# Performance work log

Measured on AMD Instinct MI355X. Metric: run time of the kernel, lower is better.

The kernel has to match this reference:

```python
import jax, jax.numpy as jnp
import numpy as np

N = 100000   # nodes
E = 1600000  # edges (avg degree 16)
D = 128      # in = hid = out dim
EPS = 1e-5   # BatchNorm eps


def setup_inputs() -> dict:
    key = jax.random.key(0)
    ks = jax.random.split(key, 14)
    x = jax.random.normal(ks[0], (N, D), dtype=jnp.float32)
    row = jax.random.randint(ks[1], (E,), 0, N, dtype=jnp.int32)
    col = jax.random.randint(ks[2], (E,), 0, N, dtype=jnp.int32)
    edge_weight = jax.random.uniform(ks[3], (E,), dtype=jnp.float32)
    s = 1.0 / np.sqrt(D)
    W0 = jax.random.uniform(ks[4], (D, D), jnp.float32, -s, s)
    b0 = jax.random.uniform(ks[5], (D,), jnp.float32, -s, s)
    W1 = jax.random.uniform(ks[6], (D, D), jnp.float32, -s, s)
    b1 = jax.random.uniform(ks[7], (D,), jnp.float32, -s, s)
    W2 = jax.random.uniform(ks[8], (D, D), jnp.float32, -s, s)
    b2 = jax.random.uniform(ks[9], (D,), jnp.float32, -s, s)
    g0 = jnp.ones((D,), jnp.float32); be0 = jnp.zeros((D,), jnp.float32)
    g1 = jnp.ones((D,), jnp.float32); be1 = jnp.zeros((D,), jnp.float32)
    return {"x": x, "edge_weight": edge_weight,
            "W0": W0, "b0": b0, "g0": g0, "be0": be0,
            "W1": W1, "b1": b1, "g1": g1, "be1": be1,
            "W2": W2, "b2": b2, "row": row, "col": col}


def _spmm(edge_weight, row, col, h):
    # (A_norm @ h) with A in COO: out[r] = sum_e w_e * h[col_e] for row_e == r
    return jax.ops.segment_sum(edge_weight[:, None] * h[col], row, num_segments=N)


def _bn(h, gamma, beta):
    # BatchNorm1d, training-mode stats (biased variance), over the node axis
    m = h.mean(axis=0)
    v = h.var(axis=0)
    return gamma * (h - m) * jax.lax.rsqrt(v + EPS) + beta


def reference(x, edge_weight, W0, b0, g0, be0, W1, b1, g1, be1, W2, b2, row, col):
    # hidden block 1: SpMM(A, Linear(h)) -> BN -> ReLU (dropout p=0)
    h = jax.nn.relu(_bn(_spmm(edge_weight, row, col, x @ W0 + b0), g0, be0))
    # hidden block 2
    h = jax.nn.relu(_bn(_spmm(edge_weight, row, col, h @ W1 + b1), g1, be1))
    # final layer: SpMM(A, Linear(h)), no BN/activation
    return _spmm(edge_weight, row, col, h @ W2 + b2)
```

## Files before the change

kernel.cpp:

```cpp
#include <hip/hip_runtime.h>
#include <cstddef>

#define DD 128
#define EPS 1e-5f

typedef short short8 __attribute__((ext_vector_type(8)));
typedef float float4v __attribute__((ext_vector_type(4)));

__device__ __forceinline__ unsigned short f2bf(float f) {
    union { float f; unsigned int u; } x; x.f = f;
    unsigned int r = x.u + 0x7fffu + ((x.u >> 16) & 1u);
    return (unsigned short)(r >> 16);
}
__device__ __forceinline__ float bfhi2f(unsigned int hi_bits) {
    union { unsigned int u; float f; } x; x.u = hi_bits;
    return x.f;
}


__global__ void hist_kernel(const int* __restrict__ row, int* __restrict__ deg, int E) {
    int e = blockIdx.x * blockDim.x + threadIdx.x;
    if (e < E) atomicAdd(&deg[row[e]], 1);
}

__global__ void scanA_kernel(const int* __restrict__ deg, int* __restrict__ tmp,
                             int* __restrict__ bsum, int n) {
    __shared__ int s[1024];
    int tid = threadIdx.x;
    int gid = blockIdx.x * 1024 + tid;
    int v = (gid < n) ? deg[gid] : 0;
    s[tid] = v;
    __syncthreads();
    for (int off = 1; off < 1024; off <<= 1) {
        int t = s[tid];
        int u = (tid >= off) ? s[tid - off] : 0;
        __syncthreads();
        s[tid] = t + u;
        __syncthreads();
    }
    if (gid < n) tmp[gid] = s[tid];
    if (tid == 1023) bsum[blockIdx.x] = s[1023];
}

__global__ void scanB_kernel(const int* __restrict__ bsum, int* __restrict__ boff,
                             int* __restrict__ row_start, int nb, int n) {
    __shared__ int s[128];
    int tid = threadIdx.x;
    int v = (tid < nb) ? bsum[tid] : 0;
    s[tid] = v;
    __syncthreads();
    for (int off = 1; off < 128; off <<= 1) {
        int t = s[tid];
        int u = (tid >= off) ? s[tid - off] : 0;
        __syncthreads();
        s[tid] = t + u;
        __syncthreads();
    }
    if (tid < nb) boff[tid] = s[tid] - v;
    if (tid == nb - 1) row_start[n] = s[tid];
}

__global__ void scanC_kernel(const int* __restrict__ deg, const int* __restrict__ tmp,
                             const int* __restrict__ boff, int* __restrict__ row_start,
                             int* __restrict__ cursor, int n) {
    int gid = blockIdx.x * 1024 + threadIdx.x;
    if (gid < n) {
        int rs = tmp[gid] - deg[gid] + boff[blockIdx.x];
        row_start[gid] = rs;
        cursor[gid] = rs;
    }
}

#define SCHUNK 2048

__global__ __launch_bounds__(256) void scatter_bucketed_kernel(
    const int* __restrict__ row, const int* __restrict__ col,
    const float* __restrict__ ew, int* __restrict__ cursor,
    unsigned long long* __restrict__ ebuf, int E, unsigned int bmagic) {
    int chunk = blockIdx.x >> 3;
    unsigned int bucket = blockIdx.x & 7;
    int base = chunk * SCHUNK + threadIdx.x;
    #pragma unroll
    for (int i = 0; i < SCHUNK / 256; ++i) {
        int e = base + i * 256;
        if (e < E) {
            int r = row[e];
            if (__umulhi((unsigned int)r, bmagic) == bucket) {
                int p = atomicAdd(&cursor[r], 1);
                unsigned long long pk = (unsigned long long)(unsigned int)col[e]
                                      | ((unsigned long long)__float_as_uint(ew[e]) << 32);
                ebuf[p] = pk;
            }
        }
    }
}


__global__ void convw_kernel(const float* __restrict__ W0, const float* __restrict__ W1,
                             const float* __restrict__ W2, unsigned short* __restrict__ T0,
                             unsigned short* __restrict__ T1, unsigned short* __restrict__ T2) {
    const float* W = (blockIdx.y == 0) ? W0 : (blockIdx.y == 1) ? W1 : W2;
    unsigned short* T = (blockIdx.y == 0) ? T0 : (blockIdx.y == 1) ? T1 : T2;
    int gid = blockIdx.x * 256 + threadIdx.x;
    int k = gid >> 7, n = gid & 127;
    T[n * DD + k] = f2bf(W[k * DD + n]);
}


__global__ __launch_bounds__(256) void gemm_mfma_f32_kernel(
    const float* __restrict__ A, const unsigned short* __restrict__ Wt,
    const float* __restrict__ bias, unsigned short* __restrict__ H, int nrows)
{
    __shared__ unsigned short Asl[64][136];
    __shared__ unsigned short Wsl[128][136];

    const int tid  = threadIdx.x;
    const int row0 = blockIdx.x * 64;

    for (int i = tid; i < 2048; i += 256) {
        int r = i >> 4, off = (i & 15) * 8;
        *(uint4*)&Wsl[r][off] = *(const uint4*)(Wt + (size_t)r * DD + off);
    }
    for (int i = tid; i < 2048; i += 256) {
        int r = i >> 5, off4 = i & 31;
        int grow = row0 + r;
        float4 v = make_float4(0.f, 0.f, 0.f, 0.f);
        if (grow < nrows)
            v = *(const float4*)(A + (size_t)grow * DD + off4 * 4);
        ushort4 p;
        p.x = f2bf(v.x); p.y = f2bf(v.y); p.z = f2bf(v.z); p.w = f2bf(v.w);
        *(ushort4*)&Asl[r][off4 * 4] = p;
    }
    __syncthreads();

    const int w = tid >> 6, lane = tid & 63;
    const int m = lane & 15, q = lane >> 4;

    short8 afr[4];
    #pragma unroll
    for (int c = 0; c < 4; ++c)
        afr[c] = *(const short8*)&Asl[w * 16 + m][c * 32 + q * 8];

    float4v acc[8];
    #pragma unroll
    for (int t = 0; t < 8; ++t) acc[t] = (float4v){0.f, 0.f, 0.f, 0.f};

    #pragma unroll
    for (int t = 0; t < 8; ++t) {
        #pragma unroll
        for (int c = 0; c < 4; ++c) {
            short8 bfr = *(const short8*)&Wsl[t * 16 + m][c * 32 + q * 8];
            acc[t] = __builtin_amdgcn_mfma_f32_16x16x32_bf16(afr[c], bfr, acc[t], 0, 0, 0);
        }
    }

    #pragma unroll
    for (int t = 0; t < 8; ++t) {
        float bv = bias[t * 16 + m];
        #pragma unroll
        for (int i = 0; i < 4; ++i)
            Asl[w * 16 + q * 4 + i][t * 16 + m] = f2bf(acc[t][i] + bv);
    }
    __syncthreads();

    for (int i = tid; i < 1024; i += 256) {
        int r = i >> 4, off = (i & 15) * 8;
        if (row0 + r < nrows)
            *(uint4*)(H + (size_t)(row0 + r) * DD + off) = *(const uint4*)&Asl[r][off];
    }
}


__global__ __launch_bounds__(256) void gemm_mfma_bf16_kernel(
    const unsigned int* __restrict__ A, const unsigned short* __restrict__ Wt,
    const float* __restrict__ bias,
    const float* __restrict__ sums, const float* __restrict__ g,
    const float* __restrict__ be,
    unsigned short* __restrict__ H, int nrows)
{
    __shared__ unsigned short Asl[64][136];
    __shared__ unsigned short Wsl[128][136];
    __shared__ float scl_s[128], sft_s[128];

    const int tid  = threadIdx.x;
    const int row0 = blockIdx.x * 64;

    if (tid < 128) {
        float inv_n = 1.0f / (float)nrows;
        float mean = sums[tid] * inv_n;
        float var = sums[128 + tid] * inv_n - mean * mean;
        float rstd = rsqrtf(var + EPS);
        float sc = g[tid] * rstd;
        scl_s[tid] = sc;
        sft_s[tid] = be[tid] - mean * sc;
    }

    for (int i = tid; i < 2048; i += 256) {
        int r = i >> 4, off = (i & 15) * 8;
        *(uint4*)&Wsl[r][off] = *(const uint4*)(Wt + (size_t)r * DD + off);
    }
    __syncthreads();

    for (int i = tid; i < 1024; i += 256) {
        int r = i >> 4, ch = (i & 15) * 8;
        int grow = row0 + r;
        uint4 u = make_uint4(0, 0, 0, 0);
        if (grow < nrows)
            u = *(const uint4*)(A + (size_t)grow * 64 + (ch >> 1));
        unsigned int uu[4] = {u.x, u.y, u.z, u.w};
        unsigned int outp[4];
        #pragma unroll
        for (int j = 0; j < 4; ++j) {
            float vx = bfhi2f(uu[j] << 16);
            float vy = bfhi2f(uu[j] & 0xffff0000u);
            int k = ch + j * 2;
            vx = fmaxf(0.f, vx * scl_s[k] + sft_s[k]);
            vy = fmaxf(0.f, vy * scl_s[k + 1] + sft_s[k + 1]);
            outp[j] = (unsigned int)f2bf(vx) | ((unsigned int)f2bf(vy) << 16);
        }
        *(uint4*)&Asl[r][ch] = *(const uint4*)outp;
    }
    __syncthreads();

    const int w = tid >> 6, lane = tid & 63;
    const int m = lane & 15, q = lane >> 4;

    short8 afr[4];
    #pragma unroll
    for (int c = 0; c < 4; ++c)
        afr[c] = *(const short8*)&Asl[w * 16 + m][c * 32 + q * 8];

    float4v acc[8];
    #pragma unroll
    for (int t = 0; t < 8; ++t) acc[t] = (float4v){0.f, 0.f, 0.f, 0.f};

    #pragma unroll
    for (int t = 0; t < 8; ++t) {
        #pragma unroll
        for (int c = 0; c < 4; ++c) {
            short8 bfr = *(const short8*)&Wsl[t * 16 + m][c * 32 + q * 8];
            acc[t] = __builtin_amdgcn_mfma_f32_16x16x32_bf16(afr[c], bfr, acc[t], 0, 0, 0);
        }
    }

    #pragma unroll
    for (int t = 0; t < 8; ++t) {
        float bv = bias[t * 16 + m];
        #pragma unroll
        for (int i = 0; i < 4; ++i)
            Asl[w * 16 + q * 4 + i][t * 16 + m] = f2bf(acc[t][i] + bv);
    }
    __syncthreads();

    for (int i = tid; i < 1024; i += 256) {
        int r = i >> 4, off = (i & 15) * 8;
        if (row0 + r < nrows)
            *(uint4*)(H + (size_t)(row0 + r) * DD + off) = *(const uint4*)&Asl[r][off];
    }
}


__global__ __launch_bounds__(256) void spmm_bf16_kernel(
    const unsigned short* __restrict__ H, const int* __restrict__ row_start,
    const unsigned long long* __restrict__ ebuf,
    float* __restrict__ Sf, unsigned int* __restrict__ Sb, int writeBF, int N)
{
    int g = threadIdx.x >> 6, lane = threadIdx.x & 63;
    int r = blockIdx.x * 4 + g;
    if (r >= N) return;
    int e0 = row_start[r], e1 = row_start[r + 1];
    const unsigned short* Hp = H + lane * 2;
    float ax = 0.f, ay = 0.f;
    int e = e0;
    for (; e + 7 < e1; e += 8) {
        unsigned long long p[8];
        #pragma unroll
        for (int j = 0; j < 8; ++j) p[j] = __builtin_nontemporal_load(&ebuf[e + j]);
        unsigned int u[8];
        #pragma unroll
        for (int j = 0; j < 8; ++j)
            u[j] = *(const unsigned int*)(Hp + (size_t)(unsigned int)p[j] * DD);
        #pragma unroll
        for (int j = 0; j < 8; ++j) {
            float wj = __uint_as_float((unsigned int)(p[j] >> 32));
            ax += wj * bfhi2f(u[j] << 16);
            ay += wj * bfhi2f(u[j] & 0xffff0000u);
        }
    }
    if (e + 3 < e1) {
        unsigned long long p[4];
        #pragma unroll
        for (int j = 0; j < 4; ++j) p[j] = __builtin_nontemporal_load(&ebuf[e + j]);
        unsigned int u[4];
        #pragma unroll
        for (int j = 0; j < 4; ++j)
            u[j] = *(const unsigned int*)(Hp + (size_t)(unsigned int)p[j] * DD);
        #pragma unroll
        for (int j = 0; j < 4; ++j) {
            float wj = __uint_as_float((unsigned int)(p[j] >> 32));
            ax += wj * bfhi2f(u[j] << 16);
            ay += wj * bfhi2f(u[j] & 0xffff0000u);
        }
        e += 4;
    }
    for (; e < e1; ++e) {
        unsigned long long p0 = __builtin_nontemporal_load(&ebuf[e]);
        unsigned int u0 = *(const unsigned int*)(Hp + (size_t)(unsigned int)p0 * DD);
        float w0 = __uint_as_float((unsigned int)(p0 >> 32));
        ax += w0 * bfhi2f(u0 << 16);
        ay += w0 * bfhi2f(u0 & 0xffff0000u);
    }
    if (writeBF) {
        unsigned int pk = (unsigned int)f2bf(ax) | ((unsigned int)f2bf(ay) << 16);
        Sb[(size_t)r * 64 + lane] = pk;
    } else {
        float2 o; o.x = ax; o.y = ay;
        *(float2*)(Sf + (size_t)r * DD + lane * 2) = o;
    }
}


__global__ void bn_stats_bf16_kernel(const unsigned int* __restrict__ Sb,
                                     float* __restrict__ sums, int n) {
    __shared__ float lsx[256], lsx2[256], lsy[256], lsy2[256];
    int tid = threadIdx.x;
    int c2 = tid & 63;
    float sx = 0.f, sx2 = 0.f, sy = 0.f, sy2 = 0.f;
    int total = n * 64;
    for (int i = blockIdx.x * 256 + tid; i < total; i += 256 * 256) {
        unsigned int u = Sb[i];
        float vx = bfhi2f(u << 16);
        float vy = bfhi2f(u & 0xffff0000u);
        sx += vx; sx2 += vx * vx;
        sy += vy; sy2 += vy * vy;
    }
    lsx[tid] = sx; lsx2[tid] = sx2; lsy[tid] = sy; lsy2[tid] = sy2;
    __syncthreads();
    if (tid < 64) {
        sx  = lsx[tid]  + lsx[tid + 64]  + lsx[tid + 128]  + lsx[tid + 192];
        sx2 = lsx2[tid] + lsx2[tid + 64] + lsx2[tid + 128] + lsx2[tid + 192];
        sy  = lsy[tid]  + lsy[tid + 64]  + lsy[tid + 128]  + lsy[tid + 192];
        sy2 = lsy2[tid] + lsy2[tid + 64] + lsy2[tid + 128] + lsy2[tid + 192];
        atomicAdd(&sums[2 * c2], sx);
        atomicAdd(&sums[2 * c2 + 1], sy);
        atomicAdd(&sums[128 + 2 * c2], sx2);
        atomicAdd(&sums[129 + 2 * c2], sy2);
    }
}


extern "C" void kernel_launch(void* const* d_in, const int* in_sizes, int n_in,
                              void* d_out, int out_size, void* d_ws, size_t ws_size,
                              hipStream_t stream) {
    const float* x   = (const float*)d_in[0];
    const float* ew  = (const float*)d_in[1];
    const float* W0  = (const float*)d_in[2];
    const float* b0  = (const float*)d_in[3];
    const float* g0  = (const float*)d_in[4];
    const float* be0 = (const float*)d_in[5];
    const float* W1  = (const float*)d_in[6];
    const float* b1  = (const float*)d_in[7];
    const float* g1  = (const float*)d_in[8];
    const float* be1 = (const float*)d_in[9];
    const float* W2  = (const float*)d_in[10];
    const float* b2  = (const float*)d_in[11];
    const int* row   = (const int*)d_in[12];
    const int* col   = (const int*)d_in[13];

    const int N = in_sizes[0] / DD;
    const int E = in_sizes[1];
    float* out = (float*)d_out;

    char* w = (char*)d_ws;
    unsigned short* H   = (unsigned short*)w; w += (size_t)N * DD * 2;
    unsigned int* Sb    = (unsigned int*)w;   w += (size_t)N * 64 * 4;
    unsigned long long* ebuf = (unsigned long long*)w; w += (size_t)E * 8;
    unsigned short* Wt0 = (unsigned short*)w; w += DD * DD * 2;
    unsigned short* Wt1 = (unsigned short*)w; w += DD * DD * 2;
    unsigned short* Wt2 = (unsigned short*)w; w += DD * DD * 2;
    float* sums         = (float*)w;          w += 256 * 4;
    int*   deg          = (int*)w;            w += (size_t)N * 4;
    int*   tmp          = (int*)w;            w += (size_t)N * 4;
    int*   cursor       = (int*)w;            w += (size_t)N * 4;
    int*   bsum         = (int*)w;            w += 128 * 4;
    int*   boff         = (int*)w;            w += 128 * 4;
    int*   row_start    = (int*)w;            w += (size_t)(N + 1) * 4;

    unsigned int bmagic = (unsigned int)(((unsigned long long)8 << 32) / (unsigned long long)N);

    hipMemsetAsync(deg, 0, (size_t)N * 4, stream);
    hist_kernel<<<(E + 255) / 256, 256, 0, stream>>>(row, deg, E);
    int NB = (N + 1023) / 1024;
    scanA_kernel<<<NB, 1024, 0, stream>>>(deg, tmp, bsum, N);
    scanB_kernel<<<1, 128, 0, stream>>>(bsum, boff, row_start, NB, N);
    scanC_kernel<<<NB, 1024, 0, stream>>>(deg, tmp, boff, row_start, cursor, N);
    int nchunks = (E + SCHUNK - 1) / SCHUNK;
    scatter_bucketed_kernel<<<nchunks * 8, 256, 0, stream>>>(row, col, ew, cursor, ebuf, E, bmagic);

    convw_kernel<<<dim3(64, 3), 256, 0, stream>>>(W0, W1, W2, Wt0, Wt1, Wt2);

    int gblocks = (N + 63) / 64;
    int sblocks = (N + 3) / 4;

    gemm_mfma_f32_kernel<<<gblocks, 256, 0, stream>>>(x, Wt0, b0, H, N);
    spmm_bf16_kernel<<<sblocks, 256, 0, stream>>>(H, row_start, ebuf, nullptr, Sb, 1, N);
    hipMemsetAsync(sums, 0, 256 * 4, stream);
    bn_stats_bf16_kernel<<<256, 256, 0, stream>>>(Sb, sums, N);

    gemm_mfma_bf16_kernel<<<gblocks, 256, 0, stream>>>(Sb, Wt1, b1, sums, g0, be0, H, N);
    spmm_bf16_kernel<<<sblocks, 256, 0, stream>>>(H, row_start, ebuf, nullptr, Sb, 1, N);
    hipMemsetAsync(sums, 0, 256 * 4, stream);
    bn_stats_bf16_kernel<<<256, 256, 0, stream>>>(Sb, sums, N);

    gemm_mfma_bf16_kernel<<<gblocks, 256, 0, stream>>>(Sb, Wt2, b2, sums, g1, be1, H, N);
    spmm_bf16_kernel<<<sblocks, 256, 0, stream>>>(H, row_start, ebuf, out, nullptr, 0, N);
}
```

Before: 630.9 us.

## Restructure SpMM: quarter-wave per edge with 16B gathers, persistent rows per wave

Each wavefront now splits into four 16-lane groups. Each group handles a different edge and gathers a full 256-byte bf16 row with uint4 loads, and partial sums are combined with cross-group shuffles. Waves also loop over a contiguous span of K rows on a fixed grid of 2048 blocks instead of one row per wave. The aim is wider, more parallel gather loads and less launch and tail overhead. In exchange it adds shuffle reductions, idle lanes on writes, and possible load imbalance when row degrees vary.

```diff
diff --git a/kernel.cpp b/kernel.cpp
--- a/kernel.cpp
+++ b/kernel.cpp
@@ -260,62 +260,115 @@
 }
 
 
-__global__ __launch_bounds__(256) void spmm_bf16_kernel(
+__global__ __launch_bounds__(256, 8) void spmm_bf16_kernel(
     const unsigned short* __restrict__ H, const int* __restrict__ row_start,
     const unsigned long long* __restrict__ ebuf,
-    float* __restrict__ Sf, unsigned int* __restrict__ Sb, int writeBF, int N)
+    float* __restrict__ Sf, unsigned int* __restrict__ Sb, int writeBF, int N, int K)
 {
-    int g = threadIdx.x >> 6, lane = threadIdx.x & 63;
-    int r = blockIdx.x * 4 + g;
-    if (r >= N) return;
-    int e0 = row_start[r], e1 = row_start[r + 1];
-    const unsigned short* Hp = H + lane * 2;
-    float ax = 0.f, ay = 0.f;
-    int e = e0;
-    for (; e + 7 < e1; e += 8) {
-        unsigned long long p[8];
-        #pragma unroll
-        for (int j = 0; j < 8; ++j) p[j] = __builtin_nontemporal_load(&ebuf[e + j]);
-        unsigned int u[8];
-        #pragma unroll
-        for (int j = 0; j < 8; ++j)
-            u[j] = *(const unsigned int*)(Hp + (size_t)(unsigned int)p[j] * DD);
+    const int lane = threadIdx.x & 63;
+    const int g = lane >> 4;
+    const int p = lane & 15;
+    const int wave = (blockIdx.x << 2) | (threadIdx.x >> 6);
+    int r0 = wave * K;
+    if (r0 >= N) return;
+    int r1 = min(N, r0 + K);
+
+    const unsigned short* Hp = H + p * 8;
+    const unsigned long long* Ep = ebuf + g;
+
+    for (int r = r0; r < r1; ++r) {
+        int e = row_start[r];
+        const int e1 = row_start[r + 1];
+        float acc[8];
+        #pragma unroll
+        for (int j = 0; j < 8; ++j) acc[j] = 0.f;
+
+        for (; e + 15 < e1; e += 16) {
+            unsigned long long pk[4];
+            #pragma unroll
+            for (int j = 0; j < 4; ++j)
+                pk[j] = __builtin_nontemporal_load(Ep + e + j * 4);
+            uint4 u[4];
+            #pragma unroll
+            for (int j = 0; j < 4; ++j)
+                u[j] = *(const uint4*)(Hp + (size_t)(unsigned int)pk[j] * DD);
+            #pragma unroll
+            for (int j = 0; j < 4; ++j) {
+                float wj = __uint_as_float((unsigned int)(pk[j] >> 32));
+                unsigned int uu[4] = {u[j].x, u[j].y, u[j].z, u[j].w};
+                #pragma unroll
+                for (int q = 0; q < 4; ++q) {
+                    acc[2 * q]     += wj * bfhi2f(uu[q] << 16);
+                    acc[2 * q + 1] += wj * bfhi2f(uu[q] & 0xffff0000u);
+                }
+            }
+        }
+        for (; e + 7 < e1; e += 8) {
+            unsigned long long pk[2];
+            #pragma unroll
+            for (int j = 0; j < 2; ++j)
+                pk[j] = __builtin_nontemporal_load(Ep + e + j * 4);
+            uint4 u[2];
+            #pragma unroll
+            for (int j = 0; j < 2; ++j)
+                u[j] = *(const uint4*)(Hp + (size_t)(unsigned int)pk[j] * DD);
+            #pragma unroll
+            for (int j = 0; j < 2; ++j) {
+                float wj = __uint_as_float((unsigned int)(pk[j] >> 32));
+                unsigned int uu[4] = {u[j].x, u[j].y, u[j].z, u[j].w};
+                #pragma unroll
+                for (int q = 0; q < 4; ++q) {
+                    acc[2 * q]     += wj * bfhi2f(uu[q] << 16);
+                    acc[2 * q + 1] += wj * bfhi2f(uu[q] & 0xffff0000u);
+                }
+            }
+        }
+        if (e + 3 < e1) {
+            unsigned long long pk = __builtin_nontemporal_load(Ep + e);
+            uint4 u = *(const uint4*)(Hp + (size_t)(unsigned int)pk * DD);
+            float wj = __uint_as_float((unsigned int)(pk >> 32));
+            unsigned int uu[4] = {u.x, u.y, u.z, u.w};
+            #pragma unroll
+            for (int q = 0; q < 4; ++q) {
+                acc[2 * q]     += wj * bfhi2f(uu[q] << 16);
+                acc[2 * q + 1] += wj * bfhi2f(uu[q] & 0xffff0000u);
+            }
+            e += 4;
+        }
+        if (e < e1) {
+            int idx = e + g;
+            unsigned long long pk = (idx < e1) ? __builtin_nontemporal_load(&ebuf[idx]) : 0ull;
+            uint4 u = *(const uint4*)(Hp + (size_t)(unsigned int)pk * DD);
+            float wj = __uint_as_float((unsigned int)(pk >> 32));
+            unsigned int uu[4] = {u.x, u.y, u.z, u.w};
+            #pragma unroll
+            for (int q = 0; q < 4; ++q) {
+                acc[2 * q]     += wj * bfhi2f(uu[q] << 16);
+                acc[2 * q + 1] += wj * bfhi2f(uu[q] & 0xffff0000u);
+            }
+        }
+
         #pragma unroll
         for (int j = 0; j < 8; ++j) {
-            float wj = __uint_as_float((unsigned int)(p[j] >> 32));
-            ax += wj * bfhi2f(u[j] << 16);
-            ay += wj * bfhi2f(u[j] & 0xffff0000u);
-        }
-    }
-    if (e + 3 < e1) {
-        unsigned long long p[4];
-        #pragma unroll
-        for (int j = 0; j < 4; ++j) p[j] = __builtin_nontemporal_load(&ebuf[e + j]);
-        unsigned int u[4];
-        #pragma unroll
-        for (int j = 0; j < 4; ++j)
-            u[j] = *(const unsigned int*)(Hp + (size_t)(unsigned int)p[j] * DD);
-        #pragma unroll
-        for (int j = 0; j < 4; ++j) {
-            float wj = __uint_as_float((unsigned int)(p[j] >> 32));
-            ax += wj * bfhi2f(u[j] << 16);
-            ay += wj * bfhi2f(u[j] & 0xffff0000u);
-        }
-        e += 4;
-    }
-    for (; e < e1; ++e) {
-        unsigned long long p0 = __builtin_nontemporal_load(&ebuf[e]);
-        unsigned int u0 = *(const unsigned int*)(Hp + (size_t)(unsigned int)p0 * DD);
-        float w0 = __uint_as_float((unsigned int)(p0 >> 32));
-        ax += w0 * bfhi2f(u0 << 16);
-        ay += w0 * bfhi2f(u0 & 0xffff0000u);
-    }
-    if (writeBF) {
-        unsigned int pk = (unsigned int)f2bf(ax) | ((unsigned int)f2bf(ay) << 16);
-        Sb[(size_t)r * 64 + lane] = pk;
-    } else {
-        float2 o; o.x = ax; o.y = ay;
-        *(float2*)(Sf + (size_t)r * DD + lane * 2) = o;
+            acc[j] += __shfl_xor(acc[j], 16);
+            acc[j] += __shfl_xor(acc[j], 32);
+        }
+
+        if (g == 0) {
+            if (writeBF) {
+                unsigned int o[4];
+                #pragma unroll
+                for (int j = 0; j < 4; ++j)
+                    o[j] = (unsigned int)f2bf(acc[2 * j])
+                         | ((unsigned int)f2bf(acc[2 * j + 1]) << 16);
+                *(uint4*)(Sb + (size_t)r * 64 + p * 4) = *(const uint4*)o;
+            } else {
+                float4 lo = make_float4(acc[0], acc[1], acc[2], acc[3]);
+                float4 hi = make_float4(acc[4], acc[5], acc[6], acc[7]);
+                *(float4*)(Sf + (size_t)r * DD + p * 8) = lo;
+                *(float4*)(Sf + (size_t)r * DD + p * 8 + 4) = hi;
+            }
+        }
     }
 }
 
@@ -400,18 +453,21 @@
     convw_kernel<<<dim3(64, 3), 256, 0, stream>>>(W0, W1, W2, Wt0, Wt1, Wt2);
 
     int gblocks = (N + 63) / 64;
-    int sblocks = (N + 3) / 4;
+
+    const int SPMM_BLOCKS = 2048;
+    const int totalWaves = SPMM_BLOCKS * 4;
+    const int K = (N + totalWaves - 1) / totalWaves;
 
     gemm_mfma_f32_kernel<<<gblocks, 256, 0, stream>>>(x, Wt0, b0, H, N);
-    spmm_bf16_kernel<<<sblocks, 256, 0, stream>>>(H, row_start, ebuf, nullptr, Sb, 1, N);
+    spmm_bf16_kernel<<<SPMM_BLOCKS, 256, 0, stream>>>(H, row_start, ebuf, nullptr, Sb, 1, N, K);
     hipMemsetAsync(sums, 0, 256 * 4, stream);
     bn_stats_bf16_kernel<<<256, 256, 0, stream>>>(Sb, sums, N);
 
     gemm_mfma_bf16_kernel<<<gblocks, 256, 0, stream>>>(Sb, Wt1, b1, sums, g0, be0, H, N);
-    spmm_bf16_kernel<<<sblocks, 256, 0, stream>>>(H, row_start, ebuf, nullptr, Sb, 1, N);
+    spmm_bf16_kernel<<<SPMM_BLOCKS, 256, 0, stream>>>(H, row_start, ebuf, nullptr, Sb, 1, N, K);
     hipMemsetAsync(sums, 0, 256 * 4, stream);
     bn_stats_bf16_kernel<<<256, 256, 0, stream>>>(Sb, sums, N);
 
     gemm_mfma_bf16_kernel<<<gblocks, 256, 0, stream>>>(Sb, Wt2, b2, sums, g1, be1, H, N);
-    spmm_bf16_kernel<<<sblocks, 256, 0, stream>>>(H, row_start, ebuf, out, nullptr, 0, N);
-}
+    spmm_bf16_kernel<<<SPMM_BLOCKS, 256, 0, stream>>>(H, row_start, ebuf, out, nullptr, 0, N, K);
+}
```

Measured after the change: 599.2 us. 1.05x faster.
